# Kernel tuning notes

Measured on AMD Instinct MI355X. Metric: run time of the kernel, lower is better.

## Reference

```python
import jax, jax.numpy as jnp
import numpy as np
from math import pi

K_MAX = 0.1   # init k
DLT_K = 0.02  # init dk
EPS = 0.1

N_IMG, N_ATOM = 32, 400000


def _dot(a, b):
    # sum over last two dims, keepdims -> shape [..., 1, 1]
    return jnp.sum(a * b, axis=(-2, -1), keepdims=True)


def _norm(a):
    return jnp.sqrt(_dot(a, a))


def setup_inputs() -> dict:
    key = jax.random.key(0)
    k1, k2, k3 = jax.random.split(key, 3)
    pos = jax.random.normal(k1, (N_IMG, N_ATOM, 3), dtype=jnp.float32)
    frc = jax.random.normal(k2, (N_IMG, N_ATOM, 3), dtype=jnp.float32)
    eng = jax.random.normal(k3, (N_IMG,), dtype=jnp.float32)
    # ensure climbing-image argmax lies in the interior (valid frc_para index)
    eng = eng.at[N_IMG // 2].add(10.0)
    return {"pos": pos, "frc": frc, "eng": eng}


def reference(pos, frc, eng):
    dtype = pos.dtype
    eng3 = eng[:, None, None]  # [N,1,1]

    # ---- spring force k per segment: [N-1,1,1] ----
    eng_ref = jnp.min(eng3) - EPS
    eng_max = jnp.max(eng3)
    eng_i = jnp.maximum(eng3[1:], eng3[:-1])
    k = K_MAX - DLT_K * (eng_max - eng_i) / (eng_max - eng_ref)
    k = jnp.where(eng_i < eng_ref, K_MAX - DLT_K, k)

    # ---- improved tangent estimation: [N-2, A, 3] ----
    tau_p = pos[1:-1] - pos[:-2]
    tau_m = pos[2:] - pos[1:-1]
    e0, e1, e2 = eng3[:-2], eng3[1:-1], eng3[2:]
    msk_pp = ((e2 > e1) & (e1 > e0)).astype(dtype)
    msk_mm = ((e2 < e1) & (e1 < e0)).astype(dtype)
    not_both = 1.0 - jnp.maximum(msk_pp, msk_mm)
    msk_p = (e2 > e1).astype(dtype) * not_both
    msk_m = (e2 < e1).astype(dtype) * not_both
    dv_max = jnp.maximum(jnp.abs(e2 - e1), jnp.abs(e0 - e1))
    dv_min = jnp.minimum(jnp.abs(e2 - e1), jnp.abs(e0 - e1))
    tau = (tau_p * msk_pp + tau_m * msk_mm
           + (tau_p * dv_max + tau_m * dv_min) * msk_p
           + (tau_p * dv_min + tau_m * dv_max) * msk_m)
    tau = tau / _norm(tau)

    # ---- NEB force decomposition ----
    frc_in = frc[1:-1]
    vecp = pos[2:] - pos[1:-1]
    vecm = pos[1:-1] - pos[:-2]
    frc_para = _dot(frc_in, tau) * tau
    spr = k[1:] * vecp - k[:-1] * vecm
    spr_para = (k[1:] * _norm(vecp) - k[:-1] * _norm(vecm)) * tau
    frc_perp = frc_in - frc_para  # uses pre-climbing frc_para (torch in-place order)
    spr_perp = spr - spr_para

    # climbing image: double parallel force at the highest-energy image
    i = jnp.argmax(eng) - 1  # eng index -> frc_para index offset (interior images)
    # torch indexes frc_para with the raw eng argmax; reproduce that indexing
    i_raw = jnp.argmax(eng)
    frc_para = frc_para.at[i_raw].multiply(2.0)

    frc_neb = spr_para - frc_para  # nudged=True

    # doubly nudged switch term
    sw = (2.0 / pi) * jnp.arctan2(_dot(frc_perp, frc_perp), _dot(spr_perp, spr_perp))
    doubly = spr_perp - _dot(spr_perp, frc_perp) * frc_perp * sw
    frc_neb = frc_neb + doubly

    out_frc = frc + jnp.pad(frc_neb, ((1, 1), (0, 0), (0, 0)))
    return out_frc
```

## Files before the change

### kernel.cpp

```cpp
#include <hip/hip_runtime.h>
#include <math.h>

#define N_IMG 32
#define N_ATOM 400000
#define NE (N_ATOM*3)
#define NE4 (NE/4)
#define KMAXC 0.1f
#define DLTKC 0.02f
#define EPSE 0.1f

#define OFF_SDD 0
#define OFF_SPM 31
#define OFF_SFP 61
#define OFF_SFM 91
#define OFF_SFF 121
#define NSUM 151
#define OFF_CO  160
#define OFF_PART 256
#define PSTRIDE 160

#define NBXP 586
#define NBX2 1172
#define NCHUNK 5

__device__ __forceinline__ float dot4(float4 a, float4 b) {
    return a.x*b.x + a.y*b.y + a.z*b.z + a.w*b.w;
}
__device__ __forceinline__ float4 sub4(float4 a, float4 b) {
    return make_float4(a.x-b.x, a.y-b.y, a.z-b.z, a.w-b.w);
}

__device__ __forceinline__ float wred_dpp(float x) {
    x += __int_as_float(__builtin_amdgcn_update_dpp(0, __float_as_int(x), 0x111, 0xf, 0xf, false));
    x += __int_as_float(__builtin_amdgcn_update_dpp(0, __float_as_int(x), 0x112, 0xf, 0xf, false));
    x += __int_as_float(__builtin_amdgcn_update_dpp(0, __float_as_int(x), 0x114, 0xf, 0xf, false));
    x += __int_as_float(__builtin_amdgcn_update_dpp(0, __float_as_int(x), 0x118, 0xf, 0xf, false));
    x += __int_as_float(__builtin_amdgcn_update_dpp(0, __float_as_int(x), 0x142, 0xa, 0xf, false));
    x += __int_as_float(__builtin_amdgcn_update_dpp(0, __float_as_int(x), 0x143, 0xc, 0xf, false));
    return x;
}

__global__ __launch_bounds__(256, 3) void eb_pass1(const float* __restrict__ pos,
                                                   const float* __restrict__ frc,
                                                   float* __restrict__ part) {
    const int c = blockIdx.y;
    const int j0 = 1 + 6 * c;
    const float4* pos4 = reinterpret_cast<const float4*>(pos);
    const float4* frc4 = reinterpret_cast<const float4*>(frc);

    float sdd[7], spm[6], sfp[6], sfm[6], sff[6];
#pragma unroll
    for (int i = 0; i < 7; ++i) sdd[i] = 0.f;
#pragma unroll
    for (int i = 0; i < 6; ++i) { spm[i] = 0.f; sfp[i] = 0.f; sfm[i] = 0.f; sff[i] = 0.f; }

    for (int t = blockIdx.x * 256 + threadIdx.x; t < NE4; t += 256 * NBXP) {
        float4 p[8], f[6];
#pragma unroll
        for (int i = 0; i < 8; ++i) p[i] = pos4[(size_t)(j0 - 1 + i) * NE4 + t];
#pragma unroll
        for (int i = 0; i < 6; ++i) f[i] = frc4[(size_t)(j0 + i) * NE4 + t];
        float4 d[7];
#pragma unroll
        for (int i = 0; i < 7; ++i) d[i] = sub4(p[i + 1], p[i]);
#pragma unroll
        for (int i = 0; i < 7; ++i) sdd[i] += dot4(d[i], d[i]);
#pragma unroll
        for (int jj = 0; jj < 6; ++jj) {
            spm[jj] += dot4(d[jj], d[jj + 1]);
            sfp[jj] += dot4(f[jj], d[jj]);
            sfm[jj] += dot4(f[jj], d[jj + 1]);
            sff[jj] += dot4(f[jj], f[jj]);
        }
    }

    float v[31];
#pragma unroll
    for (int i = 0; i < 7; ++i) v[i] = sdd[i];
#pragma unroll
    for (int i = 0; i < 6; ++i) { v[7 + i] = spm[i]; v[13 + i] = sfp[i]; v[19 + i] = sfm[i]; v[25 + i] = sff[i]; }

    __shared__ float red[4][31];
    const int wave = threadIdx.x >> 6;
    const int lane = threadIdx.x & 63;
#pragma unroll
    for (int s = 0; s < 31; ++s) {
        float r = wred_dpp(v[s]);
        if (lane == 63) red[wave][s] = r;
    }
    __syncthreads();
    const int s = threadIdx.x;
    if (s < 31) {
        float r = red[0][s] + red[1][s] + red[2][s] + red[3][s];
        int slot; bool owned = true;
        if (s < 7)       { owned = (s < 6) || (c == NCHUNK - 1); slot = OFF_SDD + (j0 - 1) + s; }
        else if (s < 13) slot = OFF_SPM + (j0 - 1) + (s - 7);
        else if (s < 19) slot = OFF_SFP + (j0 - 1) + (s - 13);
        else if (s < 25) slot = OFF_SFM + (j0 - 1) + (s - 19);
        else             slot = OFF_SFF + (j0 - 1) + (s - 25);
        if (owned) part[(size_t)blockIdx.x * PSTRIDE + slot] = r;
    }
}

__global__ __launch_bounds__(256) void eb_reduce(const float* __restrict__ part,
                                                 float* __restrict__ sums) {
    const int s = blockIdx.x;
    float acc = 0.f;
    for (int r = threadIdx.x; r < NBXP; r += 256)
        acc += part[(size_t)r * PSTRIDE + s];
    __shared__ float red[4];
    const int wave = threadIdx.x >> 6;
    const int lane = threadIdx.x & 63;
    float v = wred_dpp(acc);
    if (lane == 63) red[wave] = v;
    __syncthreads();
    if (threadIdx.x == 0) sums[s] = red[0] + red[1] + red[2] + red[3];
}

__global__ void eb_coeff(const float* __restrict__ eng,
                         const float* __restrict__ sums,
                         float* __restrict__ co) {
    const int jj = threadIdx.x;
    if (jj >= N_IMG - 2 || blockIdx.x != 0) return;
    float e[N_IMG];
    float emin = 1e30f, emax = -1e30f;
    int imax = 0;
    for (int i = 0; i < N_IMG; ++i) {
        float v = eng[i];
        e[i] = v;
        if (v < emin) emin = v;
        if (v > emax) { emax = v; imax = i; }
    }
    const float eref = emin - EPSE;
    float e0 = e[jj], e1 = e[jj + 1], e2 = e[jj + 2];
    float eim = fmaxf(e1, e0);
    float km = KMAXC - DLTKC * (emax - eim) / (emax - eref);
    if (eim < eref) km = KMAXC - DLTKC;
    float eip = fmaxf(e2, e1);
    float kp = KMAXC - DLTKC * (emax - eip) / (emax - eref);
    if (eip < eref) kp = KMAXC - DLTKC;

    float pp = (e2 > e1 && e1 > e0) ? 1.f : 0.f;
    float mm = (e2 < e1 && e1 < e0) ? 1.f : 0.f;
    float nb = 1.f - fmaxf(pp, mm);
    float mp = ((e2 > e1) ? 1.f : 0.f) * nb;
    float mq = ((e2 < e1) ? 1.f : 0.f) * nb;
    float dvmax = fmaxf(fabsf(e2 - e1), fabsf(e0 - e1));
    float dvmin = fminf(fabsf(e2 - e1), fabsf(e0 - e1));
    float a = pp + dvmax * mp + dvmin * mq;
    float b = mm + dvmin * mp + dvmax * mq;
    float Spp = sums[OFF_SDD + jj];
    float Smm = sums[OFF_SDD + jj + 1];
    float Spm = sums[OFF_SPM + jj];
    float Sfp = sums[OFF_SFP + jj];
    float Sfm = sums[OFF_SFM + jj];
    float Sff = sums[OFF_SFF + jj];
    float ntau2 = a * a * Spp + 2.f * a * b * Spm + b * b * Smm;
    float ntau = sqrtf(ntau2);
    float ta = a / ntau, tb = b / ntau;
    float fpar = ta * Sfp + tb * Sfm;
    float spar = kp * sqrtf(Smm) - km * sqrtf(Spp);
    float ffpp = Sff - fpar * fpar;
    float strau = ta * (kp * Spm - km * Spp) + tb * (kp * Smm - km * Spm);
    float Sss = kp * kp * Smm - 2.f * kp * km * Spm + km * km * Spp;
    float sspp = Sss - 2.f * spar * strau + spar * spar;
    float Ssf = kp * Sfm - km * Sfp;
    float spfp = Ssf - fpar * strau;
    float sw = (2.0f / 3.14159265358979323846f) * atan2f(ffpp, sspp);
    float cc = spfp * sw;
    float g = (jj == imax) ? 2.f : 1.f;
    float w = (cc - g) * fpar / ntau;
    co[jj]      = 1.f - cc;
    co[30 + jj] = kp + w * b;
    co[60 + jj] = w * a - km;
}

__global__ __launch_bounds__(256, 4) void eb_pass2(const float* __restrict__ pos,
                                                   const float* __restrict__ frc,
                                                   const float* __restrict__ co,
                                                   float* __restrict__ out) {
    __shared__ float A[30], B[30], C[30];
    if (threadIdx.x < 30) {
        A[threadIdx.x] = co[threadIdx.x];
        B[threadIdx.x] = co[30 + threadIdx.x];
        C[threadIdx.x] = co[60 + threadIdx.x];
    }
    __syncthreads();
    const int t = blockIdx.x * 256 + threadIdx.x;
    if (t >= NE4) return;
    const int c = blockIdx.y;
    const int j0 = 1 + 6 * c;
    const float4* pos4 = reinterpret_cast<const float4*>(pos);
    const float4* frc4 = reinterpret_cast<const float4*>(frc);
    float4* out4 = reinterpret_cast<float4*>(out);

    float4 p[8], f[6];
#pragma unroll
    for (int i = 0; i < 8; ++i) p[i] = pos4[(size_t)(j0 - 1 + i) * NE4 + t];
#pragma unroll
    for (int i = 0; i < 6; ++i) f[i] = frc4[(size_t)(j0 + i) * NE4 + t];

    if (c == 0) out4[t] = frc4[t];
    if (c == NCHUNK - 1) {
        size_t i31 = (size_t)31 * NE4 + t;
        out4[i31] = frc4[i31];
    }

    float4 d[7];
#pragma unroll
    for (int i = 0; i < 7; ++i) d[i] = sub4(p[i + 1], p[i]);
#pragma unroll
    for (int jj = 0; jj < 6; ++jj) {
        const int j = j0 + jj;
        const int g = j - 1;
        float ca = A[g], cb = B[g], cd = C[g];
        float4 o;
        o.x = ca * f[jj].x + cb * d[jj + 1].x + cd * d[jj].x;
        o.y = ca * f[jj].y + cb * d[jj + 1].y + cd * d[jj].y;
        o.z = ca * f[jj].z + cb * d[jj + 1].z + cd * d[jj].z;
        o.w = ca * f[jj].w + cb * d[jj + 1].w + cd * d[jj].w;
        out4[(size_t)j * NE4 + t] = o;
    }
}

extern "C" void kernel_launch(void* const* d_in, const int* in_sizes, int n_in,
                              void* d_out, int out_size, void* d_ws, size_t ws_size,
                              hipStream_t stream) {
    const float* pos = (const float*)d_in[0];
    const float* frc = (const float*)d_in[1];
    const float* eng = (const float*)d_in[2];
    float* out = (float*)d_out;
    float* ws = (float*)d_ws;
    float* sums = ws;
    float* co   = ws + OFF_CO;
    float* part = ws + OFF_PART;

    eb_pass1<<<dim3(NBXP, NCHUNK), 256, 0, stream>>>(pos, frc, part);
    eb_reduce<<<NSUM, 256, 0, stream>>>(part, sums);
    eb_coeff<<<1, 64, 0, stream>>>(eng, sums, co);
    eb_pass2<<<dim3(NBX2, NCHUNK), 256, 0, stream>>>(pos, frc, co, out);
}
```

Before: 420.1 us.

## Fuse reduction, coefficient and output passes into one cooperative kernel

Replaces four kernel launches (partial reduction, final reduce, coefficient solve, output pass) with one cooperative persistent kernel that uses grid-wide syncs. Per-block partial sums are combined with atomicAdd into a small global array instead of a separate reduce kernel, and every block recomputes the per-segment coefficients into shared memory. This removes launch gaps and the partial-sum buffer round trip. In exchange it adds grid-sync overhead, floating-point atomics with nondeterministic ordering, a block count capped by occupancy, and redundant coefficient math in every block.

```diff
diff --git a/kernel.cpp b/kernel.cpp
--- a/kernel.cpp
+++ b/kernel.cpp
@@ -1,5 +1,8 @@
 #include <hip/hip_runtime.h>
+#include <hip/hip_cooperative_groups.h>
 #include <math.h>
+
+namespace cg = cooperative_groups;
 
 #define N_IMG 32
 #define N_ATOM 400000
@@ -9,19 +12,15 @@
 #define DLTKC 0.02f
 #define EPSE 0.1f
 
+#define NSUM 151
 #define OFF_SDD 0
 #define OFF_SPM 31
 #define OFF_SFP 61
 #define OFF_SFM 91
 #define OFF_SFF 121
-#define NSUM 151
-#define OFF_CO  160
-#define OFF_PART 256
-#define PSTRIDE 160
-
-#define NBXP 586
-#define NBX2 1172
+
 #define NCHUNK 5
+#define MAXBLK 2040
 
 __device__ __forceinline__ float dot4(float4 a, float4 b) {
     return a.x*b.x + a.y*b.y + a.z*b.z + a.w*b.w;
@@ -40,21 +39,30 @@
     return x;
 }
 
-__global__ __launch_bounds__(256, 3) void eb_pass1(const float* __restrict__ pos,
-                                                   const float* __restrict__ frc,
-                                                   float* __restrict__ part) {
-    const int c = blockIdx.y;
+__global__ __launch_bounds__(256) void eb_fused(const float* __restrict__ pos,
+                                                const float* __restrict__ frc,
+                                                const float* __restrict__ eng,
+                                                float* __restrict__ out,
+                                                float* __restrict__ sums,
+                                                int xstride) {
+    cg::grid_group gg = cg::this_grid();
+    const int b = blockIdx.x;
+    const int c = b % NCHUNK;
+    const int xb = b / NCHUNK;
     const int j0 = 1 + 6 * c;
     const float4* pos4 = reinterpret_cast<const float4*>(pos);
     const float4* frc4 = reinterpret_cast<const float4*>(frc);
 
+    if (b == 0 && threadIdx.x < NSUM) sums[threadIdx.x] = 0.f;
+    gg.sync();
+
     float sdd[7], spm[6], sfp[6], sfm[6], sff[6];
 #pragma unroll
     for (int i = 0; i < 7; ++i) sdd[i] = 0.f;
 #pragma unroll
     for (int i = 0; i < 6; ++i) { spm[i] = 0.f; sfp[i] = 0.f; sfm[i] = 0.f; sff[i] = 0.f; }
 
-    for (int t = blockIdx.x * 256 + threadIdx.x; t < NE4; t += 256 * NBXP) {
+    for (int t = xb * 256 + threadIdx.x; t < NE4; t += xstride * 256) {
         float4 p[8], f[6];
 #pragma unroll
         for (int i = 0; i < 8; ++i) p[i] = pos4[(size_t)(j0 - 1 + i) * NE4 + t];
@@ -81,145 +89,118 @@
     for (int i = 0; i < 6; ++i) { v[7 + i] = spm[i]; v[13 + i] = sfp[i]; v[19 + i] = sfm[i]; v[25 + i] = sff[i]; }
 
     __shared__ float red[4][31];
-    const int wave = threadIdx.x >> 6;
-    const int lane = threadIdx.x & 63;
-#pragma unroll
-    for (int s = 0; s < 31; ++s) {
-        float r = wred_dpp(v[s]);
-        if (lane == 63) red[wave][s] = r;
+    {
+        const int wave = threadIdx.x >> 6;
+        const int lane = threadIdx.x & 63;
+#pragma unroll
+        for (int s = 0; s < 31; ++s) {
+            float r = wred_dpp(v[s]);
+            if (lane == 63) red[wave][s] = r;
+        }
     }
     __syncthreads();
-    const int s = threadIdx.x;
-    if (s < 31) {
-        float r = red[0][s] + red[1][s] + red[2][s] + red[3][s];
-        int slot; bool owned = true;
-        if (s < 7)       { owned = (s < 6) || (c == NCHUNK - 1); slot = OFF_SDD + (j0 - 1) + s; }
-        else if (s < 13) slot = OFF_SPM + (j0 - 1) + (s - 7);
-        else if (s < 19) slot = OFF_SFP + (j0 - 1) + (s - 13);
-        else if (s < 25) slot = OFF_SFM + (j0 - 1) + (s - 19);
-        else             slot = OFF_SFF + (j0 - 1) + (s - 25);
-        if (owned) part[(size_t)blockIdx.x * PSTRIDE + slot] = r;
-    }
-}
-
-__global__ __launch_bounds__(256) void eb_reduce(const float* __restrict__ part,
-                                                 float* __restrict__ sums) {
-    const int s = blockIdx.x;
-    float acc = 0.f;
-    for (int r = threadIdx.x; r < NBXP; r += 256)
-        acc += part[(size_t)r * PSTRIDE + s];
-    __shared__ float red[4];
-    const int wave = threadIdx.x >> 6;
-    const int lane = threadIdx.x & 63;
-    float v = wred_dpp(acc);
-    if (lane == 63) red[wave] = v;
+    {
+        const int s = threadIdx.x;
+        if (s < 31) {
+            float r = red[0][s] + red[1][s] + red[2][s] + red[3][s];
+            int slot; bool owned = true;
+            if (s < 7)       { owned = (s < 6) || (c == NCHUNK - 1); slot = OFF_SDD + (j0 - 1) + s; }
+            else if (s < 13) slot = OFF_SPM + (j0 - 1) + (s - 7);
+            else if (s < 19) slot = OFF_SFP + (j0 - 1) + (s - 13);
+            else if (s < 25) slot = OFF_SFM + (j0 - 1) + (s - 19);
+            else             slot = OFF_SFF + (j0 - 1) + (s - 25);
+            if (owned) atomicAdd(&sums[slot], r);
+        }
+    }
+    __threadfence();
+    gg.sync();
+
+    __shared__ float Ac[30], Bc[30], Cc[30];
+    if (threadIdx.x < 30) {
+        const int jj = threadIdx.x;
+        volatile const float* vs = sums;
+        float e[N_IMG];
+        float emin = 1e30f, emax = -1e30f;
+        int imax = 0;
+        for (int i = 0; i < N_IMG; ++i) {
+            float vv = eng[i];
+            e[i] = vv;
+            if (vv < emin) emin = vv;
+            if (vv > emax) { emax = vv; imax = i; }
+        }
+        const float eref = emin - EPSE;
+        float e0 = e[jj], e1 = e[jj + 1], e2 = e[jj + 2];
+        float eim = fmaxf(e1, e0);
+        float km = KMAXC - DLTKC * (emax - eim) / (emax - eref);
+        if (eim < eref) km = KMAXC - DLTKC;
+        float eip = fmaxf(e2, e1);
+        float kp = KMAXC - DLTKC * (emax - eip) / (emax - eref);
+        if (eip < eref) kp = KMAXC - DLTKC;
+
+        float pp = (e2 > e1 && e1 > e0) ? 1.f : 0.f;
+        float mm = (e2 < e1 && e1 < e0) ? 1.f : 0.f;
+        float nb = 1.f - fmaxf(pp, mm);
+        float mp = ((e2 > e1) ? 1.f : 0.f) * nb;
+        float mq = ((e2 < e1) ? 1.f : 0.f) * nb;
+        float dvmax = fmaxf(fabsf(e2 - e1), fabsf(e0 - e1));
+        float dvmin = fminf(fabsf(e2 - e1), fabsf(e0 - e1));
+        float a = pp + dvmax * mp + dvmin * mq;
+        float bb = mm + dvmin * mp + dvmax * mq;
+        float Spp = vs[OFF_SDD + jj];
+        float Smm = vs[OFF_SDD + jj + 1];
+        float Spm = vs[OFF_SPM + jj];
+        float Sfp = vs[OFF_SFP + jj];
+        float Sfm = vs[OFF_SFM + jj];
+        float Sff = vs[OFF_SFF + jj];
+        float ntau2 = a * a * Spp + 2.f * a * bb * Spm + bb * bb * Smm;
+        float ntau = sqrtf(ntau2);
+        float ta = a / ntau, tb = bb / ntau;
+        float fpar = ta * Sfp + tb * Sfm;
+        float spar = kp * sqrtf(Smm) - km * sqrtf(Spp);
+        float ffpp = Sff - fpar * fpar;
+        float strau = ta * (kp * Spm - km * Spp) + tb * (kp * Smm - km * Spm);
+        float Sss = kp * kp * Smm - 2.f * kp * km * Spm + km * km * Spp;
+        float sspp = Sss - 2.f * spar * strau + spar * spar;
+        float Ssf = kp * Sfm - km * Sfp;
+        float spfp = Ssf - fpar * strau;
+        float sw = (2.0f / 3.14159265358979323846f) * atan2f(ffpp, sspp);
+        float cc = spfp * sw;
+        float g = (jj == imax) ? 2.f : 1.f;
+        float w = (cc - g) * fpar / ntau;
+        Ac[jj] = 1.f - cc;
+        Bc[jj] = kp + w * bb;
+        Cc[jj] = w * a - km;
+    }
     __syncthreads();
-    if (threadIdx.x == 0) sums[s] = red[0] + red[1] + red[2] + red[3];
-}
-
-__global__ void eb_coeff(const float* __restrict__ eng,
-                         const float* __restrict__ sums,
-                         float* __restrict__ co) {
-    const int jj = threadIdx.x;
-    if (jj >= N_IMG - 2 || blockIdx.x != 0) return;
-    float e[N_IMG];
-    float emin = 1e30f, emax = -1e30f;
-    int imax = 0;
-    for (int i = 0; i < N_IMG; ++i) {
-        float v = eng[i];
-        e[i] = v;
-        if (v < emin) emin = v;
-        if (v > emax) { emax = v; imax = i; }
-    }
-    const float eref = emin - EPSE;
-    float e0 = e[jj], e1 = e[jj + 1], e2 = e[jj + 2];
-    float eim = fmaxf(e1, e0);
-    float km = KMAXC - DLTKC * (emax - eim) / (emax - eref);
-    if (eim < eref) km = KMAXC - DLTKC;
-    float eip = fmaxf(e2, e1);
-    float kp = KMAXC - DLTKC * (emax - eip) / (emax - eref);
-    if (eip < eref) kp = KMAXC - DLTKC;
-
-    float pp = (e2 > e1 && e1 > e0) ? 1.f : 0.f;
-    float mm = (e2 < e1 && e1 < e0) ? 1.f : 0.f;
-    float nb = 1.f - fmaxf(pp, mm);
-    float mp = ((e2 > e1) ? 1.f : 0.f) * nb;
-    float mq = ((e2 < e1) ? 1.f : 0.f) * nb;
-    float dvmax = fmaxf(fabsf(e2 - e1), fabsf(e0 - e1));
-    float dvmin = fminf(fabsf(e2 - e1), fabsf(e0 - e1));
-    float a = pp + dvmax * mp + dvmin * mq;
-    float b = mm + dvmin * mp + dvmax * mq;
-    float Spp = sums[OFF_SDD + jj];
-    float Smm = sums[OFF_SDD + jj + 1];
-    float Spm = sums[OFF_SPM + jj];
-    float Sfp = sums[OFF_SFP + jj];
-    float Sfm = sums[OFF_SFM + jj];
-    float Sff = sums[OFF_SFF + jj];
-    float ntau2 = a * a * Spp + 2.f * a * b * Spm + b * b * Smm;
-    float ntau = sqrtf(ntau2);
-    float ta = a / ntau, tb = b / ntau;
-    float fpar = ta * Sfp + tb * Sfm;
-    float spar = kp * sqrtf(Smm) - km * sqrtf(Spp);
-    float ffpp = Sff - fpar * fpar;
-    float strau = ta * (kp * Spm - km * Spp) + tb * (kp * Smm - km * Spm);
-    float Sss = kp * kp * Smm - 2.f * kp * km * Spm + km * km * Spp;
-    float sspp = Sss - 2.f * spar * strau + spar * spar;
-    float Ssf = kp * Sfm - km * Sfp;
-    float spfp = Ssf - fpar * strau;
-    float sw = (2.0f / 3.14159265358979323846f) * atan2f(ffpp, sspp);
-    float cc = spfp * sw;
-    float g = (jj == imax) ? 2.f : 1.f;
-    float w = (cc - g) * fpar / ntau;
-    co[jj]      = 1.f - cc;
-    co[30 + jj] = kp + w * b;
-    co[60 + jj] = w * a - km;
-}
-
-__global__ __launch_bounds__(256, 4) void eb_pass2(const float* __restrict__ pos,
-                                                   const float* __restrict__ frc,
-                                                   const float* __restrict__ co,
-                                                   float* __restrict__ out) {
-    __shared__ float A[30], B[30], C[30];
-    if (threadIdx.x < 30) {
-        A[threadIdx.x] = co[threadIdx.x];
-        B[threadIdx.x] = co[30 + threadIdx.x];
-        C[threadIdx.x] = co[60 + threadIdx.x];
-    }
-    __syncthreads();
-    const int t = blockIdx.x * 256 + threadIdx.x;
-    if (t >= NE4) return;
-    const int c = blockIdx.y;
-    const int j0 = 1 + 6 * c;
-    const float4* pos4 = reinterpret_cast<const float4*>(pos);
-    const float4* frc4 = reinterpret_cast<const float4*>(frc);
+
     float4* out4 = reinterpret_cast<float4*>(out);
-
-    float4 p[8], f[6];
-#pragma unroll
-    for (int i = 0; i < 8; ++i) p[i] = pos4[(size_t)(j0 - 1 + i) * NE4 + t];
-#pragma unroll
-    for (int i = 0; i < 6; ++i) f[i] = frc4[(size_t)(j0 + i) * NE4 + t];
-
-    if (c == 0) out4[t] = frc4[t];
-    if (c == NCHUNK - 1) {
-        size_t i31 = (size_t)31 * NE4 + t;
-        out4[i31] = frc4[i31];
-    }
-
-    float4 d[7];
-#pragma unroll
-    for (int i = 0; i < 7; ++i) d[i] = sub4(p[i + 1], p[i]);
-#pragma unroll
-    for (int jj = 0; jj < 6; ++jj) {
-        const int j = j0 + jj;
-        const int g = j - 1;
-        float ca = A[g], cb = B[g], cd = C[g];
-        float4 o;
-        o.x = ca * f[jj].x + cb * d[jj + 1].x + cd * d[jj].x;
-        o.y = ca * f[jj].y + cb * d[jj + 1].y + cd * d[jj].y;
-        o.z = ca * f[jj].z + cb * d[jj + 1].z + cd * d[jj].z;
-        o.w = ca * f[jj].w + cb * d[jj + 1].w + cd * d[jj].w;
-        out4[(size_t)j * NE4 + t] = o;
+    for (int t = xb * 256 + threadIdx.x; t < NE4; t += xstride * 256) {
+        float4 p[8], f[6];
+#pragma unroll
+        for (int i = 0; i < 8; ++i) p[i] = pos4[(size_t)(j0 - 1 + i) * NE4 + t];
+#pragma unroll
+        for (int i = 0; i < 6; ++i) f[i] = frc4[(size_t)(j0 + i) * NE4 + t];
+
+        if (c == 0) out4[t] = frc4[t];
+        if (c == NCHUNK - 1) {
+            size_t i31 = (size_t)31 * NE4 + t;
+            out4[i31] = frc4[i31];
+        }
+
+        float4 d[7];
+#pragma unroll
+        for (int i = 0; i < 7; ++i) d[i] = sub4(p[i + 1], p[i]);
+#pragma unroll
+        for (int jj = 0; jj < 6; ++jj) {
+            const int g = j0 + jj - 1;
+            float ca = Ac[g], cb = Bc[g], cd = Cc[g];
+            float4 o;
+            o.x = ca * f[jj].x + cb * d[jj + 1].x + cd * d[jj].x;
+            o.y = ca * f[jj].y + cb * d[jj + 1].y + cd * d[jj].y;
+            o.z = ca * f[jj].z + cb * d[jj + 1].z + cd * d[jj].z;
+            o.w = ca * f[jj].w + cb * d[jj + 1].w + cd * d[jj].w;
+            out4[(size_t)(j0 + jj) * NE4 + t] = o;
+        }
     }
 }
 
@@ -230,13 +211,22 @@
     const float* frc = (const float*)d_in[1];
     const float* eng = (const float*)d_in[2];
     float* out = (float*)d_out;
-    float* ws = (float*)d_ws;
-    float* sums = ws;
-    float* co   = ws + OFF_CO;
-    float* part = ws + OFF_PART;
-
-    eb_pass1<<<dim3(NBXP, NCHUNK), 256, 0, stream>>>(pos, frc, part);
-    eb_reduce<<<NSUM, 256, 0, stream>>>(part, sums);
-    eb_coeff<<<1, 64, 0, stream>>>(eng, sums, co);
-    eb_pass2<<<dim3(NBX2, NCHUNK), 256, 0, stream>>>(pos, frc, co, out);
-}
+    float* sums = (float*)d_ws;
+
+    static int nblk = 0;
+    if (nblk == 0) {
+        int perCU = 0;
+        hipOccupancyMaxActiveBlocksPerMultiprocessor(&perCU, (const void*)eb_fused, 256, 0);
+        if (perCU < 1) perCU = 1;
+        long cap = (long)perCU * 256;
+        if (cap > MAXBLK) cap = MAXBLK;
+        nblk = (int)(cap / NCHUNK) * NCHUNK;
+        if (nblk < NCHUNK) nblk = NCHUNK;
+    }
+    int xstride = nblk / NCHUNK;
+
+    void* args[] = { (void*)&pos, (void*)&frc, (void*)&eng,
+                     (void*)&out, (void*)&sums, (void*)&xstride };
+    hipLaunchCooperativeKernel((const void*)eb_fused, dim3(nblk), dim3(256),
+                               args, 0, stream);
+}
```

Measured after the change: 587.5 us. 39.8% more time.
